# Kernel optimization log

Hardware: AMD Instinct MI355X
Metric: run time of the kernel (lower is better)

## Reference

```python
import jax, jax.numpy as jnp
import numpy as np

A, M, KA, KB = 100000, 200000, 6, 5  # atoms, messages, agraph width, bgraph width
D, DB, H = 256, 256, 256             # atom embed, bond embed, hidden
DEPTH, ATOMS, BONDS = 4, 120, 4


def setup_inputs() -> dict:
    key = jax.random.key(0)
    ks = jax.random.split(key, 14)
    f32 = jnp.float32

    def lin(k, o, i):
        s = 1.0 / np.sqrt(i)
        return jax.random.uniform(k, (o, i), f32, -s, s)

    return dict(
        E_a=jax.random.normal(ks[0], (ATOMS, D), f32) * 0.1,
        E_b=jax.random.normal(ks[1], (BONDS, DB), f32) * 0.1,
        Wz_w=lin(ks[2], H, D + DB + H), Wz_b=jnp.zeros((H,), f32),
        Wr_w=lin(ks[3], H, D + DB),
        Ur_w=lin(ks[4], H, H), Ur_b=jnp.zeros((H,), f32),
        Wh_w=lin(ks[5], H, D + DB + H), Wh_b=jnp.zeros((H,), f32),
        O1_w=lin(ks[6], H, D + H), O1_b=jnp.zeros((H,), f32),
        O2_w=lin(ks[7], H, H), O2_b=jnp.zeros((H,), f32),
        fnode=jax.random.randint(ks[8], (A,), 0, ATOMS),
        fmess_src=jax.random.randint(ks[9], (M,), 0, A),
        fmess_bond=jax.random.randint(ks[10], (M,), 0, BONDS),
        agraph=jax.random.randint(ks[11], (A, KA), 0, M),
        bgraph=jax.random.randint(ks[12], (M, KB), 0, M),
        depth=DEPTH,
    )


def reference(E_a, E_b, Wz_w, Wz_b, Wr_w, Ur_w, Ur_b, Wh_w, Wh_b,
              O1_w, O1_b, O2_w, O2_b,
              fnode, fmess_src, fmess_bond, agraph, bgraph, depth):
    # embed_graph: atom features + message input features
    hnode = E_a[fnode]                                           # [A, D]
    x = jnp.concatenate([hnode[fmess_src], E_b[fmess_bond]], -1)  # [M, D+DB]

    m = x.shape[0]
    h = jnp.zeros((m, Wz_b.shape[0]), x.dtype)                   # [M, H]
    mask = jnp.ones((m, 1), x.dtype).at[0].set(0.0)              # msg 0 = padding
    wr_x = x @ Wr_w.T                                            # loop-invariant

    # GRU message passing (JTNN-style), depthG iterations
    for _ in range(depth):
        h_nei = h[bgraph]                                        # [M, KB, H] gather
        sum_h = h_nei.sum(axis=1)
        z = jax.nn.sigmoid(jnp.concatenate([x, sum_h], -1) @ Wz_w.T + Wz_b)
        r = jax.nn.sigmoid(wr_x[:, None, :] + h_nei @ Ur_w.T + Ur_b)
        sum_gated = (r * h_nei).sum(axis=1)
        pre_h = jnp.tanh(jnp.concatenate([x, sum_gated], -1) @ Wh_w.T + Wh_b)
        h = ((1.0 - z) * sum_h + z * pre_h) * mask

    # mpn tail: gather-sum neighbor messages per atom, concat, outputAtom MLP
    mess_nei = h[agraph].sum(axis=1)                             # [A, H]
    nv = jnp.concatenate([hnode, mess_nei], axis=-1)             # [A, D+H]
    out = jax.nn.relu(nv @ O1_w.T + O1_b) @ O2_w.T + O2_b        # [A, H]
    return out
```

## Files before the change

kernel.cpp:

```cpp
#include <hip/hip_runtime.h>

#define MM 200000
#define AA 100000
#define KA 6
#define KB 5
#define NATOM 120
#define NBOND 4
#define NC (NATOM*NBOND)
#define HH 256
#define HU_LD 512

typedef unsigned short ushort_t;
typedef __attribute__((ext_vector_type(8))) short bf16x8;
typedef __attribute__((ext_vector_type(8))) unsigned short u16x8;
typedef __attribute__((ext_vector_type(4))) float f32x4;
typedef __attribute__((ext_vector_type(4))) unsigned int u32x4;

#define SBAR() __builtin_amdgcn_sched_barrier(0)

#define OFF_Ea   0
#define OFF_Eb   30720
#define OFF_Wz   31744
#define OFF_Wzb  228352
#define OFF_Wr   228608
#define OFF_Ur   359680
#define OFF_Urb  425216
#define OFF_Wh   425472
#define OFF_Whb  622080
#define OFF_O1   622336
#define OFF_O1b  753408
#define OFF_O2   753664
#define OFF_O2b  819200
#define W_TOTAL  819456

__device__ ushort_t g_hu0[MM*HU_LD];
__device__ ushort_t g_hu1[MM*HU_LD];
__device__ ushort_t g_trb[NC*HH];
__device__ float    g_tz[NC*HH];
__device__ float    g_th[NC*HH];
__device__ float    g_to1[NATOM*HH];
__device__ int      g_cidx[MM];
__device__ ushort_t c_w[W_TOTAL];
__device__ int      g_isf32;

__device__ inline float bf2f(ushort_t u){ return __uint_as_float(((unsigned)u)<<16); }
__device__ inline ushort_t f2bf(float f){
  unsigned u = __float_as_uint(f);
  unsigned r = (u + 0x7FFFu + ((u>>16)&1u)) >> 16;
  return (ushort_t)r;
}
__device__ inline float sigm(float x){
  return __builtin_amdgcn_rcpf(1.0f + __expf(-x));
}
__device__ inline float tanh_f(float x){
  float ax = fabsf(x);
  float e = __expf(-2.0f*ax);
  float t = (1.0f - e) * __builtin_amdgcn_rcpf(1.0f + e);
  return copysignf(t, x);
}
__device__ inline int sidx(int row, int col){ return row*256 + (col ^ ((row&7)<<3)); }

__device__ inline bf16x8 ldsA(const ushort_t* tile, int m0, int lane, int k0){
  int row = m0 + (lane & 15);
  int col = k0 + 8*(lane>>4);
  return *(const bf16x8*)(tile + sidx(row, col));
}
__device__ inline bf16x8 ldgB(const ushort_t* W, int ldw, int koff, int n0, int lane, int k0){
  int n = n0 + (lane & 15);
  int k = koff + k0 + 8*(lane>>4);
  return *(const bf16x8*)(W + n*ldw + k);
}
__device__ inline f32x4 mfma16(bf16x8 a, bf16x8 b, f32x4 c){
  return __builtin_amdgcn_mfma_f32_16x16x32_bf16(a, b, c, 0, 0, 0);
}
__device__ inline void st16(ushort_t* p, const ushort_t* lds_src){
  *(u32x4*)p = *(const u32x4*)lds_src;
}

__global__ __launch_bounds__(256) void k_detect(const ushort_t* Ea_raw){
  __shared__ int sbad;
  if (threadIdx.x == 0) sbad = 0;
  __syncthreads();
  float v = bf2f(Ea_raw[2*threadIdx.x]);
  float av = fabsf(v);
  int bad = (av > 1e4f) || (av != 0.0f && av < 1e-30f);
  atomicAdd(&sbad, bad);
  __syncthreads();
  if (threadIdx.x == 0) g_isf32 = (sbad > 64) ? 1 : 0;
}

__global__ __launch_bounds__(256) void k_convert(
    const void* Ea, const void* Eb, const void* Wz, const void* Wzb,
    const void* Wr, const void* Ur, const void* Urb, const void* Wh,
    const void* Whb, const void* O1, const void* O1b, const void* O2,
    const void* O2b)
{
  int idx = blockIdx.x*256 + threadIdx.x;
  if (idx >= W_TOTAL) return;
  const void* src; int j;
  if      (idx < OFF_Eb)  { src = Ea;  j = idx - OFF_Ea; }
  else if (idx < OFF_Wz)  { src = Eb;  j = idx - OFF_Eb; }
  else if (idx < OFF_Wzb) { src = Wz;  j = idx - OFF_Wz; }
  else if (idx < OFF_Wr)  { src = Wzb; j = idx - OFF_Wzb; }
  else if (idx < OFF_Ur)  { src = Wr;  j = idx - OFF_Wr; }
  else if (idx < OFF_Urb) { src = Ur;  j = idx - OFF_Ur; }
  else if (idx < OFF_Wh)  { src = Urb; j = idx - OFF_Urb; }
  else if (idx < OFF_Whb) { src = Wh;  j = idx - OFF_Wh; }
  else if (idx < OFF_O1)  { src = Whb; j = idx - OFF_Whb; }
  else if (idx < OFF_O1b) { src = O1;  j = idx - OFF_O1; }
  else if (idx < OFF_O2)  { src = O1b; j = idx - OFF_O1b; }
  else if (idx < OFF_O2b) { src = O2;  j = idx - OFF_O2; }
  else                    { src = O2b; j = idx - OFF_O2b; }
  ushort_t v;
  if (g_isf32) v = f2bf(((const float*)src)[j]);
  else         v = ((const ushort_t*)src)[j];
  c_w[idx] = v;
}

__global__ __launch_bounds__(256) void k_tables()
{
  const ushort_t* Ea  = c_w + OFF_Ea;
  const ushort_t* Eb  = c_w + OFF_Eb;
  int b = blockIdx.x, o = threadIdx.x;
  if (b < 3*NC) {
    int t = b / NC, c = b % NC, a = c >> 2, bd = c & 3;
    const ushort_t* W; const ushort_t* bias; int ldw;
    if (t == 0)      { W = c_w + OFF_Wr; bias = c_w + OFF_Urb; ldw = 512; }
    else if (t == 1) { W = c_w + OFF_Wz; bias = c_w + OFF_Wzb; ldw = 768; }
    else             { W = c_w + OFF_Wh; bias = c_w + OFF_Whb; ldw = 768; }
    float acc = bf2f(bias[o]);
    const ushort_t* wrow = W + o*ldw;
    for (int d = 0; d < 256; d++) acc += bf2f(Ea[a*256+d]) * bf2f(wrow[d]);
    for (int d = 0; d < 256; d++) acc += bf2f(Eb[bd*256+d]) * bf2f(wrow[256+d]);
    if (t == 0)      g_trb[c*256 + o] = f2bf(acc);
    else if (t == 1) g_tz[c*256 + o] = acc;
    else             g_th[c*256 + o] = acc;
  } else {
    int a = b - 3*NC;
    float acc = bf2f(c_w[OFF_O1b + o]);
    const ushort_t* wrow = c_w + OFF_O1 + o*512;
    for (int d = 0; d < 256; d++) acc += bf2f(Ea[a*256+d]) * bf2f(wrow[d]);
    g_to1[a*256 + o] = acc;
  }
}

__global__ __launch_bounds__(256) void k_cidx(const int* fnode, const int* fsrc, const int* fbond){
  int m = blockIdx.x*256 + threadIdx.x;
  if (m >= MM) return;
  g_cidx[m] = fnode[fsrc[m]]*4 + fbond[m];
}

__global__ __launch_bounds__(256) void k_iter0(){
  __shared__ __align__(16) ushort_t sT[64*256];
  const ushort_t* Ur = c_w + OFF_Ur;
  ushort_t* hu = g_hu0;
  int base = blockIdx.x * 64;
  int t = threadIdx.x;
  {
    int row = t >> 2, cb = (t & 3) * 64;
    int m = base + row;
    int c = g_cidx[m];
    float msk = (m != 0) ? 1.0f : 0.0f;
    #pragma unroll
    for (int e = 0; e < 64; e += 4){
      int col = cb + e;
      float4 tz = *(const float4*)(g_tz + c*256 + col);
      float4 th = *(const float4*)(g_th + c*256 + col);
      ushort_t h0 = f2bf(msk * sigm(tz.x) * tanh_f(th.x));
      ushort_t h1 = f2bf(msk * sigm(tz.y) * tanh_f(th.y));
      ushort_t h2 = f2bf(msk * sigm(tz.z) * tanh_f(th.z));
      ushort_t h3 = f2bf(msk * sigm(tz.w) * tanh_f(th.w));
      ushort4 hv = make_ushort4(h0,h1,h2,h3);
      *(ushort4*)(hu + (size_t)m*HU_LD + col) = hv;
      *(ushort4*)(sT + sidx(row, col)) = hv;
    }
  }
  __syncthreads();
  int w = t >> 6, lane = t & 63, n0w = w*64, ln = lane & 15, hi = lane >> 4;
  f32x4 acc[4][4];
  #pragma unroll
  for (int i=0;i<4;i++)
    #pragma unroll
    for (int j=0;j<4;j++) acc[i][j] = (f32x4){0.f,0.f,0.f,0.f};
  for (int kt = 0; kt < 8; kt++){
    int k0 = kt*32;
    bf16x8 aF[4], bF[4];
    #pragma unroll
    for (int i=0;i<4;i++) aF[i] = ldsA(sT, i*16, lane, k0);
    #pragma unroll
    for (int i=0;i<4;i++) bF[i] = ldgB(Ur, 256, 0, n0w + i*16, lane, k0);
    #pragma unroll
    for (int mi=0;mi<4;mi++)
      #pragma unroll
      for (int ni=0;ni<4;ni++) acc[mi][ni] = mfma16(aF[mi], bF[ni], acc[mi][ni]);
  }
  __syncthreads();
  #pragma unroll
  for (int mi=0;mi<4;mi++)
    #pragma unroll
    for (int ni=0;ni<4;ni++){
      int col = n0w + ni*16 + ln;
      #pragma unroll
      for (int r=0;r<4;r++){
        int rowl = mi*16 + hi*4 + r;
        sT[sidx(rowl, col)] = f2bf(acc[mi][ni][r]);
      }
    }
  __syncthreads();
  {
    #pragma unroll
    for (int it = 0; it < 8; it++){
      int flat = it*2048 + t*8;
      int row = flat >> 8, col = flat & 255;
      st16(hu + (size_t)(base+row)*HU_LD + 256 + col, sT + sidx(row, col));
    }
  }
}

__global__ __attribute__((amdgpu_flat_work_group_size(256,256), amdgpu_waves_per_eu(4,4)))
void k_fused(const int* __restrict__ bgraph, int rd, int last){
  __shared__ __align__(16) ushort_t sA[32*256];
  __shared__ __align__(16) ushort_t sB[32*256];
  __shared__ int sC[32];
  __shared__ int sJ[32*KB];
  const ushort_t* __restrict__ hup = rd ? g_hu1 : g_hu0;
  ushort_t* hun = rd ? g_hu0 : g_hu1;
  const ushort_t* Wz = c_w + OFF_Wz;
  const ushort_t* Wh = c_w + OFF_Wh;
  const ushort_t* Ur = c_w + OFF_Ur;
  int base = blockIdx.x*32, t = threadIdx.x;
  int w = t>>6, lane = t&63;
  int sub = lane & 31, half = lane >> 5;

  if (t < 32)  sC[t] = g_cidx[base + t];
  if (t < 32*KB) sJ[t] = bgraph[base*KB + t];
  __syncthreads();

  auto issue = [&](int p, bf16x8 (&hv)[KB], bf16x8 (&uv)[KB], bf16x8& trv){
    int row = w*8 + 2*p + half;
    trv = *(const bf16x8*)(g_trb + sC[row]*256 + sub*8);
    #pragma unroll
    for (int k = 0; k < KB; k++){
      const ushort_t* rp = hup + (size_t)sJ[row*KB + k]*HU_LD + sub*8;
      hv[k] = *(const bf16x8*)(rp);
      uv[k] = *(const bf16x8*)(rp + 256);
    }
  };
  auto process = [&](int p, bf16x8 (&hv)[KB], bf16x8 (&uv)[KB], bf16x8& trv){
    int row = w*8 + 2*p + half;
    float tre[8];
    #pragma unroll
    for (int e = 0; e < 8; e++) tre[e] = bf2f((ushort_t)trv[e]);
    float sh[8] = {0,0,0,0,0,0,0,0};
    float sg[8] = {0,0,0,0,0,0,0,0};
    #pragma unroll
    for (int k = 0; k < KB; k++){
      #pragma unroll
      for (int e = 0; e < 8; e++){
        float h = bf2f((ushort_t)hv[k][e]);
        float r = sigm(tre[e] + bf2f((ushort_t)uv[k][e]));
        sh[e] += h;
        sg[e] += r*h;
      }
    }
    u16x8 ph, pg;
    #pragma unroll
    for (int e = 0; e < 8; e++){ ph[e] = f2bf(sh[e]); pg[e] = f2bf(sg[e]); }
    *(u16x8*)(sA + sidx(row, sub*8)) = ph;
    *(u16x8*)(sB + sidx(row, sub*8)) = pg;
  };
  {
    bf16x8 h0[KB], u0[KB], h1[KB], u1[KB];
    bf16x8 t0v, t1v;
    issue(0, h0, u0, t0v);
    issue(1, h1, u1, t1v);
    SBAR();
    process(0, h0, u0, t0v);
    issue(2, h0, u0, t0v);
    SBAR();
    process(1, h1, u1, t1v);
    issue(3, h1, u1, t1v);
    SBAR();
    process(2, h0, u0, t0v);
    process(3, h1, u1, t1v);
  }
  __syncthreads();

  int n0w = w*64, ln = lane&15, hi = lane>>4;
  f32x4 accz[2][4], acch[2][4];
  #pragma unroll
  for (int i=0;i<2;i++)
    #pragma unroll
    for (int j=0;j<4;j++){ accz[i][j]=(f32x4){0,0,0,0}; acch[i][j]=(f32x4){0,0,0,0}; }
  for (int kt = 0; kt < 8; kt++){
    int k0 = kt*32;
    bf16x8 aF[2], bF[4];
    aF[0] = ldsA(sA, 0, lane, k0);
    aF[1] = ldsA(sA, 16, lane, k0);
    #pragma unroll
    for (int i=0;i<4;i++) bF[i] = ldgB(Wz, 768, 512, n0w + i*16, lane, k0);
    #pragma unroll
    for (int mi=0;mi<2;mi++)
      #pragma unroll
      for (int ni=0;ni<4;ni++) accz[mi][ni] = mfma16(aF[mi], bF[ni], accz[mi][ni]);
  }
  for (int kt = 0; kt < 8; kt++){
    int k0 = kt*32;
    bf16x8 aF[2], bF[4];
    aF[0] = ldsA(sB, 0, lane, k0);
    aF[1] = ldsA(sB, 16, lane, k0);
    #pragma unroll
    for (int i=0;i<4;i++) bF[i] = ldgB(Wh, 768, 512, n0w + i*16, lane, k0);
    #pragma unroll
    for (int mi=0;mi<2;mi++)
      #pragma unroll
      for (int ni=0;ni<4;ni++) acch[mi][ni] = mfma16(aF[mi], bF[ni], acch[mi][ni]);
  }
  __syncthreads();

  #pragma unroll
  for (int mi=0;mi<2;mi++)
    #pragma unroll
    for (int ni=0;ni<4;ni++){
      int col = n0w + ni*16 + ln;
      #pragma unroll
      for (int r=0;r<4;r++){
        int rowl = mi*16 + hi*4 + r;
        int rowg = base + rowl;
        int c = sC[rowl];
        float shv = bf2f(sA[sidx(rowl, col)]);
        float z  = sigm(g_tz[c*256+col] + accz[mi][ni][r]);
        float ph = tanh_f(g_th[c*256+col] + acch[mi][ni][r]);
        float hn = (1.0f - z)*shv + z*ph;
        if (rowg == 0) hn = 0.f;
        sB[sidx(rowl,col)] = f2bf(hn);
      }
    }
  __syncthreads();

  if (!last){
    f32x4 accu[2][4];
    #pragma unroll
    for (int i=0;i<2;i++)
      #pragma unroll
      for (int j=0;j<4;j++) accu[i][j]=(f32x4){0,0,0,0};
    for (int kt = 0; kt < 8; kt++){
      int k0 = kt*32;
      bf16x8 aF[2], bF[4];
      aF[0] = ldsA(sB, 0, lane, k0);
      aF[1] = ldsA(sB, 16, lane, k0);
      #pragma unroll
      for (int i=0;i<4;i++) bF[i] = ldgB(Ur, 256, 0, n0w + i*16, lane, k0);
      #pragma unroll
      for (int mi=0;mi<2;mi++)
        #pragma unroll
        for (int ni=0;ni<4;ni++) accu[mi][ni] = mfma16(aF[mi], bF[ni], accu[mi][ni]);
    }
    #pragma unroll
    for (int mi=0;mi<2;mi++)
      #pragma unroll
      for (int ni=0;ni<4;ni++){
        int col = n0w + ni*16 + ln;
        #pragma unroll
        for (int r=0;r<4;r++){
          int rowl = mi*16 + hi*4 + r;
          sA[sidx(rowl, col)] = f2bf(accu[mi][ni][r]);
        }
      }
    __syncthreads();
  }

  {
    #pragma unroll
    for (int it = 0; it < 4; it++){
      int flat = it*2048 + t*8;
      int row = flat >> 8, col = flat & 255;
      size_t rb = (size_t)(base+row)*HU_LD;
      st16(hun + rb + col, sB + sidx(row, col));
      if (!last) st16(hun + rb + 256 + col, sA + sidx(row, col));
    }
  }
}

__global__ __attribute__((amdgpu_flat_work_group_size(256,256), amdgpu_waves_per_eu(4,4)))
void k_tail(const int* agraph, const int* fnode, void* out_v, int rd){
  __shared__ __align__(16) ushort_t sT[64*256];
  const ushort_t* __restrict__ hup = rd ? g_hu1 : g_hu0;
  const ushort_t* O1  = c_w + OFF_O1;
  const ushort_t* O2  = c_w + OFF_O2;
  const ushort_t* O2b = c_w + OFF_O2b;
  int base = blockIdx.x*64, t = threadIdx.x;
  int w = t>>6, lane = t&63;
  int sub = lane & 31, half = lane >> 5;

  auto tissue = [&](int p, bf16x8 (&hv)[KA]){
    int rowl = w*16 + 2*p + half;
    int a = base + rowl;
    int aa = (a < AA) ? a : 0;
    #pragma unroll
    for (int k = 0; k < KA; k++){
      int j = agraph[aa*KA + k];
      hv[k] = *(const bf16x8*)(hup + (size_t)j*HU_LD + sub*8);
    }
  };
  auto tproc = [&](int p, bf16x8 (&hv)[KA]){
    int rowl = w*16 + 2*p + half;
    float s[8] = {0,0,0,0,0,0,0,0};
    #pragma unroll
    for (int k = 0; k < KA; k++)
      #pragma unroll
      for (int e = 0; e < 8; e++) s[e] += bf2f((ushort_t)hv[k][e]);
    u16x8 pk;
    #pragma unroll
    for (int e = 0; e < 8; e++) pk[e] = f2bf(s[e]);
    *(u16x8*)(sT + sidx(rowl, sub*8)) = pk;
  };
  {
    bf16x8 b0[KA], b1[KA];
    tissue(0, b0); tissue(1, b1);
    SBAR();
    tproc(0, b0);  tissue(2, b0);
    SBAR();
    tproc(1, b1);  tissue(3, b1);
    SBAR();
    tproc(2, b0);  tissue(4, b0);
    SBAR();
    tproc(3, b1);  tissue(5, b1);
    SBAR();
    tproc(4, b0);  tissue(6, b0);
    SBAR();
    tproc(5, b1);  tissue(7, b1);
    SBAR();
    tproc(6, b0);
    tproc(7, b1);
  }
  __syncthreads();
  int n0w = w*64, ln = lane&15, hi = lane>>4;
  f32x4 acc[4][4];
  #pragma unroll
  for (int i=0;i<4;i++)
    #pragma unroll
    for (int j=0;j<4;j++) acc[i][j]=(f32x4){0,0,0,0};
  for (int kt = 0; kt < 8; kt++){
    int k0 = kt*32;
    bf16x8 aF[4], bF[4];
    #pragma unroll
    for (int i=0;i<4;i++) aF[i] = ldsA(sT, i*16, lane, k0);
    #pragma unroll
    for (int i=0;i<4;i++) bF[i] = ldgB(O1, 512, 256, n0w + i*16, lane, k0);
    #pragma unroll
    for (int mi=0;mi<4;mi++)
      #pragma unroll
      for (int ni=0;ni<4;ni++) acc[mi][ni] = mfma16(aF[mi], bF[ni], acc[mi][ni]);
  }
  __syncthreads();
  #pragma unroll
  for (int mi=0;mi<4;mi++)
    #pragma unroll
    for (int ni=0;ni<4;ni++){
      int col = n0w + ni*16 + ln;
      #pragma unroll
      for (int r=0;r<4;r++){
        int rowl = mi*16 + hi*4 + r;
        int a = base + rowl;
        int tt = (a < AA) ? fnode[a] : 0;
        float pre = g_to1[tt*256+col] + acc[mi][ni][r];
        sT[sidx(rowl,col)] = f2bf(fmaxf(pre, 0.f));
      }
    }
  __syncthreads();
  f32x4 acco[4][4];
  #pragma unroll
  for (int i=0;i<4;i++)
    #pragma unroll
    for (int j=0;j<4;j++) acco[i][j]=(f32x4){0,0,0,0};
  for (int kt = 0; kt < 8; kt++){
    int k0 = kt*32;
    bf16x8 aF[4], bF[4];
    #pragma unroll
    for (int i=0;i<4;i++) aF[i] = ldsA(sT, i*16, lane, k0);
    #pragma unroll
    for (int i=0;i<4;i++) bF[i] = ldgB(O2, 256, 0, n0w + i*16, lane, k0);
    #pragma unroll
    for (int mi=0;mi<4;mi++)
      #pragma unroll
      for (int ni=0;ni<4;ni++) acco[mi][ni] = mfma16(aF[mi], bF[ni], acco[mi][ni]);
  }
  int isf32 = g_isf32;
  #pragma unroll
  for (int mi=0;mi<4;mi++)
    #pragma unroll
    for (int ni=0;ni<4;ni++){
      int col = n0w + ni*16 + ln;
      float bias = bf2f(O2b[col]);
      #pragma unroll
      for (int r=0;r<4;r++){
        int rowg = base + mi*16 + hi*4 + r;
        if (rowg < AA){
          float v = acco[mi][ni][r] + bias;
          if (isf32) ((float*)out_v)[(size_t)rowg*256 + col] = v;
          else       ((ushort_t*)out_v)[(size_t)rowg*256 + col] = f2bf(v);
        }
      }
    }
}

extern "C" void kernel_launch(void* const* d_in, const int* in_sizes, int n_in,
                              void* d_out, int out_size, void* d_ws, size_t ws_size,
                              hipStream_t stream) {
  const int* fnode = (const int*)d_in[13];
  const int* fsrc  = (const int*)d_in[14];
  const int* fbond = (const int*)d_in[15];
  const int* agraph = (const int*)d_in[16];
  const int* bgraph = (const int*)d_in[17];

  k_detect<<<1, 256, 0, stream>>>((const ushort_t*)d_in[0]);
  k_convert<<<(W_TOTAL + 255)/256, 256, 0, stream>>>(
      d_in[0], d_in[1], d_in[2], d_in[3], d_in[4], d_in[5], d_in[6],
      d_in[7], d_in[8], d_in[9], d_in[10], d_in[11], d_in[12]);
  k_tables<<<3*NC + NATOM, 256, 0, stream>>>();
  k_cidx<<<(MM + 255)/256, 256, 0, stream>>>(fnode, fsrc, fbond);
  k_iter0<<<MM/64, 256, 0, stream>>>();
  k_fused<<<MM/32, 256, 0, stream>>>(bgraph, 0, 0);
  k_fused<<<MM/32, 256, 0, stream>>>(bgraph, 1, 0);
  k_fused<<<MM/32, 256, 0, stream>>>(bgraph, 0, 1);
  k_tail<<<(AA + 63)/64, 256, 0, stream>>>(agraph, fnode, (void*)d_out, 1);
}
```

Measured before the change: 1.657 ms.

## Replace iteration-0 kernel with per-combination lookup table for first GRU step

After the first GRU step, each message's hidden state depends only on its (atom type, bond type) combination, so h and h·Ur^T are computed once for the 480 combinations plus a zero padding row. The first fused iteration then gathers from this small table by remapping neighbour indices through g_cidx. This removes the full 200k-row iter0 pass: its writes of h and Ur products, and its MFMA GEMM. In exchange it adds an extra dependent index load per neighbour, and it changes launch-bound attributes on k_fused and k_tail.

```diff
diff --git a/kernel.cpp b/kernel.cpp
--- a/kernel.cpp
+++ b/kernel.cpp
@@ -35,6 +35,7 @@
 
 __device__ ushort_t g_hu0[MM*HU_LD];
 __device__ ushort_t g_hu1[MM*HU_LD];
+__device__ ushort_t g_tab[481*HU_LD];
 __device__ ushort_t g_trb[NC*HH];
 __device__ float    g_tz[NC*HH];
 __device__ float    g_th[NC*HH];
@@ -150,80 +151,31 @@
   g_cidx[m] = fnode[fsrc[m]]*4 + fbond[m];
 }
 
-__global__ __launch_bounds__(256) void k_iter0(){
-  __shared__ __align__(16) ushort_t sT[64*256];
-  const ushort_t* Ur = c_w + OFF_Ur;
-  ushort_t* hu = g_hu0;
-  int base = blockIdx.x * 64;
-  int t = threadIdx.x;
-  {
-    int row = t >> 2, cb = (t & 3) * 64;
-    int m = base + row;
-    int c = g_cidx[m];
-    float msk = (m != 0) ? 1.0f : 0.0f;
-    #pragma unroll
-    for (int e = 0; e < 64; e += 4){
-      int col = cb + e;
-      float4 tz = *(const float4*)(g_tz + c*256 + col);
-      float4 th = *(const float4*)(g_th + c*256 + col);
-      ushort_t h0 = f2bf(msk * sigm(tz.x) * tanh_f(th.x));
-      ushort_t h1 = f2bf(msk * sigm(tz.y) * tanh_f(th.y));
-      ushort_t h2 = f2bf(msk * sigm(tz.z) * tanh_f(th.z));
-      ushort_t h3 = f2bf(msk * sigm(tz.w) * tanh_f(th.w));
-      ushort4 hv = make_ushort4(h0,h1,h2,h3);
-      *(ushort4*)(hu + (size_t)m*HU_LD + col) = hv;
-      *(ushort4*)(sT + sidx(row, col)) = hv;
-    }
-  }
-  __syncthreads();
-  int w = t >> 6, lane = t & 63, n0w = w*64, ln = lane & 15, hi = lane >> 4;
-  f32x4 acc[4][4];
-  #pragma unroll
-  for (int i=0;i<4;i++)
-    #pragma unroll
-    for (int j=0;j<4;j++) acc[i][j] = (f32x4){0.f,0.f,0.f,0.f};
-  for (int kt = 0; kt < 8; kt++){
-    int k0 = kt*32;
-    bf16x8 aF[4], bF[4];
-    #pragma unroll
-    for (int i=0;i<4;i++) aF[i] = ldsA(sT, i*16, lane, k0);
-    #pragma unroll
-    for (int i=0;i<4;i++) bF[i] = ldgB(Ur, 256, 0, n0w + i*16, lane, k0);
-    #pragma unroll
-    for (int mi=0;mi<4;mi++)
-      #pragma unroll
-      for (int ni=0;ni<4;ni++) acc[mi][ni] = mfma16(aF[mi], bF[ni], acc[mi][ni]);
-  }
-  __syncthreads();
-  #pragma unroll
-  for (int mi=0;mi<4;mi++)
-    #pragma unroll
-    for (int ni=0;ni<4;ni++){
-      int col = n0w + ni*16 + ln;
-      #pragma unroll
-      for (int r=0;r<4;r++){
-        int rowl = mi*16 + hi*4 + r;
-        sT[sidx(rowl, col)] = f2bf(acc[mi][ni][r]);
-      }
-    }
-  __syncthreads();
-  {
-    #pragma unroll
-    for (int it = 0; it < 8; it++){
-      int flat = it*2048 + t*8;
-      int row = flat >> 8, col = flat & 255;
-      st16(hu + (size_t)(base+row)*HU_LD + 256 + col, sT + sidx(row, col));
-    }
-  }
-}
-
-__global__ __attribute__((amdgpu_flat_work_group_size(256,256), amdgpu_waves_per_eu(4,4)))
-void k_fused(const int* __restrict__ bgraph, int rd, int last){
+__global__ __launch_bounds__(256) void k_tab0(){
+  __shared__ ushort_t sh[256];
+  int b = blockIdx.x, o = threadIdx.x;
+  if (b == 480){
+    g_tab[(size_t)b*HU_LD + o] = 0;
+    g_tab[(size_t)b*HU_LD + 256 + o] = 0;
+    return;
+  }
+  float h = sigm(g_tz[b*256+o]) * tanh_f(g_th[b*256+o]);
+  ushort_t hb = f2bf(h);
+  g_tab[(size_t)b*HU_LD + o] = hb;
+  sh[o] = hb;
+  __syncthreads();
+  const ushort_t* ur = c_w + OFF_Ur + o*256;
+  float acc = 0.f;
+  for (int d = 0; d < 256; d++) acc += bf2f(sh[d]) * bf2f(ur[d]);
+  g_tab[(size_t)b*HU_LD + 256 + o] = f2bf(acc);
+}
+
+__global__ __launch_bounds__(256,4) void k_fused(const int* __restrict__ bgraph, int rd, int tbl, int last){
   __shared__ __align__(16) ushort_t sA[32*256];
   __shared__ __align__(16) ushort_t sB[32*256];
   __shared__ int sC[32];
   __shared__ int sJ[32*KB];
-  const ushort_t* __restrict__ hup = rd ? g_hu1 : g_hu0;
+  const ushort_t* __restrict__ hup = tbl ? g_tab : (rd ? g_hu1 : g_hu0);
   ushort_t* hun = rd ? g_hu0 : g_hu1;
   const ushort_t* Wz = c_w + OFF_Wz;
   const ushort_t* Wh = c_w + OFF_Wh;
@@ -233,7 +185,10 @@
   int sub = lane & 31, half = lane >> 5;
 
   if (t < 32)  sC[t] = g_cidx[base + t];
-  if (t < 32*KB) sJ[t] = bgraph[base*KB + t];
+  if (t < 32*KB){
+    int j = bgraph[base*KB + t];
+    sJ[t] = tbl ? ((j == 0) ? 480 : g_cidx[j]) : j;
+  }
   __syncthreads();
 
   auto issue = [&](int p, bf16x8 (&hv)[KB], bf16x8 (&uv)[KB], bf16x8& trv){
@@ -382,8 +337,8 @@
   }
 }
 
-__global__ __attribute__((amdgpu_flat_work_group_size(256,256), amdgpu_waves_per_eu(4,4)))
-void k_tail(const int* agraph, const int* fnode, void* out_v, int rd){
+__global__ __launch_bounds__(256) void k_tail(const int* agraph, const int* fnode,
+                                              void* out_v, int rd){
   __shared__ __align__(16) ushort_t sT[64*256];
   const ushort_t* __restrict__ hup = rd ? g_hu1 : g_hu0;
   const ushort_t* O1  = c_w + OFF_O1;
@@ -520,9 +475,9 @@
       d_in[7], d_in[8], d_in[9], d_in[10], d_in[11], d_in[12]);
   k_tables<<<3*NC + NATOM, 256, 0, stream>>>();
   k_cidx<<<(MM + 255)/256, 256, 0, stream>>>(fnode, fsrc, fbond);
-  k_iter0<<<MM/64, 256, 0, stream>>>();
-  k_fused<<<MM/32, 256, 0, stream>>>(bgraph, 0, 0);
-  k_fused<<<MM/32, 256, 0, stream>>>(bgraph, 1, 0);
-  k_fused<<<MM/32, 256, 0, stream>>>(bgraph, 0, 1);
-  k_tail<<<(AA + 63)/64, 256, 0, stream>>>(agraph, fnode, (void*)d_out, 1);
-}
+  k_tab0<<<481, 256, 0, stream>>>();
+  k_fused<<<MM/32, 256, 0, stream>>>(bgraph, 1, 1, 0);
+  k_fused<<<MM/32, 256, 0, stream>>>(bgraph, 0, 0, 0);
+  k_fused<<<MM/32, 256, 0, stream>>>(bgraph, 1, 0, 1);
+  k_tail<<<(AA + 63)/64, 256, 0, stream>>>(agraph, fnode, (void*)d_out, 0);
+}
```

Measured after the change: 1.484 ms. 10.5% less time.
